# Optimization experiments

Measured on AMD Instinct MI355X. Metric: run time of the kernel, lower is better.

The kernel has to match this reference:

```python
import jax, jax.numpy as jnp
import numpy as np

B, N, K = 4, 2048, 32
CIN, COUT, M = 64, 64, 8
HID = 16
EPS = 1e-5


def setup_inputs() -> dict:
    key = jax.random.key(0)
    ks = jax.random.split(key, 12)
    inp = {
        "grouped_xyz": jax.random.normal(ks[0], (B, 3, N, K), jnp.float32),
        "grouped_dist": jax.random.uniform(ks[1], (B, N, K), jnp.float32),
        "grouped_norm": jax.random.normal(ks[2], (B, 3, N, K), jnp.float32),
        "grouped_angle": jax.random.normal(ks[3], (B, 3, N, K), jnp.float32),
        "feature": jax.random.normal(ks[4], (B, CIN, N, K), jnp.float32),
        # scorenet conv1 (14->16, 1x1, no bias) + BN params
        "w1": jax.random.normal(ks[5], (HID, 14), jnp.float32) * (2.0 / 14) ** 0.5,
        "g1": jnp.ones((HID,), jnp.float32),
        "b1": jnp.zeros((HID,), jnp.float32),
        # scorenet conv2 (16->M, 1x1, with bias, no last bn)
        "w2": jax.random.normal(ks[6], (M, HID), jnp.float32) * (2.0 / HID) ** 0.5,
        "bias2": jnp.zeros((M,), jnp.float32),
        # weight bank: kaiming on (M, CIN, COUT) -> permute -> (CIN, M*COUT)
        "weightbank": (jax.random.normal(ks[7], (M, CIN, COUT), jnp.float32)
                       * (2.0 / CIN) ** 0.5).transpose(1, 0, 2).reshape(CIN, M * COUT),
        # output BN params
        "gamma": jnp.ones((COUT,), jnp.float32),
        "beta": jnp.zeros((COUT,), jnp.float32),
    }
    return inp


def _bn_train(x, gamma, beta):
    # BatchNorm2d in training mode: stats over (B, N, K) per channel (axis=1)
    mean = x.mean(axis=(0, 2, 3), keepdims=True)
    var = x.var(axis=(0, 2, 3), keepdims=True)
    xn = (x - mean) * jax.lax.rsqrt(var + EPS)
    return xn * gamma[None, :, None, None] + beta[None, :, None, None]


def _softmax_one(x, axis):
    # exp(x) / (1 + sum exp(x)), numerically stable
    m = jax.lax.stop_gradient(x.max(axis=axis, keepdims=True))
    e = jnp.exp(x - m)
    return e / (e.sum(axis=axis, keepdims=True) + jnp.exp(-m))


def reference(grouped_xyz, grouped_dist, grouped_norm, grouped_angle, feature,
              w1, g1, b1, w2, bias2, weightbank, gamma, beta):
    # geometric feature build -> (B, 14, N, K)
    center_norm = jnp.broadcast_to(grouped_norm[..., :1], grouped_norm.shape)
    norm_diff = grouped_norm - center_norm
    norm_ed = jnp.linalg.norm(norm_diff, axis=1, keepdims=True)   # (B,1,N,K)
    xyz_ed = jnp.linalg.norm(grouped_xyz, axis=1, keepdims=True)  # (B,1,N,K)
    xyz = jnp.concatenate(
        [grouped_xyz, xyz_ed, grouped_norm, norm_diff, norm_ed, grouped_angle],
        axis=1) / (1.0 + grouped_dist[:, None, :, :])

    # scorenet: 1x1 conv + BN + ReLU, then 1x1 conv + bias, softmax_one over channels
    h = jnp.einsum('oc,bcnk->bonk', w1, xyz)
    h = jax.nn.relu(_bn_train(h, g1, b1))
    s = jnp.einsum('oc,bcnk->bonk', w2, h) + bias2[None, :, None, None]
    scores = _softmax_one(s, axis=1)                 # (B, M, N, K)
    scores = scores.transpose(0, 2, 3, 1)            # (B, N, K, M)

    # weight-bank matmul + score-weighted combine
    feat = feature.transpose(0, 2, 3, 1)             # (B, N, K, CIN)
    out = (feat @ weightbank).reshape(B, N, K, M, COUT)
    out = jnp.einsum('bnkm,bnkmo->bnko', scores, out)  # (B, N, K, COUT)
    out = out.transpose(0, 3, 1, 2)                  # (B, COUT, N, K)

    out = _bn_train(out, gamma, beta)
    return jax.nn.relu(out)
```

## Files before the change

### kernel.cpp

```cpp
#include <hip/hip_runtime.h>
#include <hip/hip_bf16.h>
#include <math.h>

namespace {

constexpr int Kn   = 32;
constexpr int CIN  = 64;
constexpr int COUT = 64;
constexpr int Mn   = 8;
constexpr int HIDn = 16;
constexpr int NK   = 65536;
constexpr int PTOT = 262144;
constexpr float EPSf = 1e-5f;

constexpr int WS_SUM1 = 0;
constexpr int WS_SQ1  = 16;
constexpr int WS_SC1  = 32;
constexpr int WS_SH1  = 48;
constexpr int WS_SUM2 = 64;
constexpr int WS_SQ2  = 128;
constexpr int WS_SC2  = 192;
constexpr int WS_SH2  = 256;
constexpr int WS_TOT  = 320;

typedef short bf16x8 __attribute__((ext_vector_type(8)));
typedef float f32x4  __attribute__((ext_vector_type(4)));

__device__ __forceinline__ short f2bf(float f) {
  union { __hip_bfloat16 h; unsigned short u; } cv;
  cv.h = __float2bfloat16(f);
  return (short)cv.u;
}

__device__ __forceinline__ void geom_h(
    const float* __restrict__ xyz, const float* __restrict__ dist,
    const float* __restrict__ nrm, const float* __restrict__ ang,
    const float* __restrict__ w1, int b, int rem, float h[HIDn]) {
  const int cbase = rem & ~(Kn - 1);
  float x[14];
  const float invd = 1.0f / (1.0f + dist[b * NK + rem]);
  float xe = 0.f, ne = 0.f;
#pragma unroll
  for (int d = 0; d < 3; ++d) {
    const int base = (b * 3 + d) * NK;
    const float gx = xyz[base + rem];
    const float gn = nrm[base + rem];
    const float cn = nrm[base + cbase];
    const float ga = ang[base + rem];
    const float nd = gn - cn;
    x[d] = gx; x[4 + d] = gn; x[7 + d] = nd; x[11 + d] = ga;
    xe += gx * gx; ne += nd * nd;
  }
  x[3]  = sqrtf(xe);
  x[10] = sqrtf(ne);
#pragma unroll
  for (int i = 0; i < 14; ++i) x[i] *= invd;
#pragma unroll
  for (int o = 0; o < HIDn; ++o) {
    float s = 0.f;
#pragma unroll
    for (int c = 0; c < 14; ++c) s = fmaf(w1[o * 14 + c], x[c], s);
    h[o] = s;
  }
}

__global__ __launch_bounds__(512) void k0_zero(float* __restrict__ ws) {
  const int t = threadIdx.x;
  if (t < WS_TOT) ws[t] = 0.f;
}

__global__ __launch_bounds__(256) void k1_stats1(
    const float* __restrict__ xyz, const float* __restrict__ dist,
    const float* __restrict__ nrm, const float* __restrict__ ang,
    const float* __restrict__ w1, float* __restrict__ ws) {
  const int pos = blockIdx.x * 256 + threadIdx.x;
  const int b   = pos >> 16;
  const int rem = pos & (NK - 1);
  float h[HIDn];
  geom_h(xyz, dist, nrm, ang, w1, b, rem, h);

  float v[32];
#pragma unroll
  for (int i = 0; i < 16; ++i) { v[i] = h[i]; v[16 + i] = h[i] * h[i]; }
#pragma unroll
  for (int off = 32; off >= 1; off >>= 1) {
#pragma unroll
    for (int i = 0; i < 32; ++i) v[i] += __shfl_xor(v[i], off);
  }
  const int lane = threadIdx.x & 63;
  const int wid  = threadIdx.x >> 6;
  float mv = 0.f;
#pragma unroll
  for (int i = 0; i < 32; ++i) { if (lane == i) mv = v[i]; }
  __shared__ float red[4][32];
  if (lane < 32) red[wid][lane] = mv;
  __syncthreads();
  if (threadIdx.x < 32) {
    const float tot = red[0][threadIdx.x] + red[1][threadIdx.x] +
                      red[2][threadIdx.x] + red[3][threadIdx.x];
    atomicAdd(&ws[WS_SUM1 + threadIdx.x], tot);
  }
}

__global__ __launch_bounds__(64) void k2_fin1(const float* __restrict__ g1,
                                              const float* __restrict__ b1,
                                              float* __restrict__ ws) {
  const int c = threadIdx.x;
  if (c >= HIDn) return;
  const float inv  = 1.0f / (float)PTOT;
  const float mean = ws[WS_SUM1 + c] * inv;
  const float var  = ws[WS_SQ1 + c] * inv - mean * mean;
  const float sc   = g1[c] * rsqrtf(var + EPSf);
  ws[WS_SC1 + c] = sc;
  ws[WS_SH1 + c] = b1[c] - mean * sc;
}

__global__ __launch_bounds__(512, 4) void k3_mfma(
    const float* __restrict__ xyz, const float* __restrict__ dist,
    const float* __restrict__ nrm, const float* __restrict__ ang,
    const float* __restrict__ feature, const float* __restrict__ w1,
    const float* __restrict__ w2, const float* __restrict__ bias2,
    const float* __restrict__ wb, float* __restrict__ ws,
    float* __restrict__ out) {
  __shared__ short lds_b[16 * 4 * 64 * 8];
  __shared__ float red[8][128];

  const int tid = threadIdx.x;
  const int l   = tid & 63;
  const int w   = tid >> 6;
  const int g   = l >> 4;
  const int row = l & 15;

#pragma unroll
  for (int ff = 0; ff < 8; ++ff) {
    const int fi   = w * 8 + ff;
    const int t    = fi >> 2;
    const int colt = fi & 3;
    const int c    = t * 4 + g;
    const int o    = colt * 16 + row;
    bf16x8 frag;
#pragma unroll
    for (int j = 0; j < 8; ++j) frag[j] = f2bf(wb[c * 512 + j * 64 + o]);
    *reinterpret_cast<bf16x8*>(&lds_b[(fi * 64 + l) * 8]) = frag;
  }

  const int pos0 = blockIdx.x * 256 + w * 32;
  const int myp  = pos0 + (l & 31);
  const int b    = myp >> 16;
  const int rem  = myp & (NK - 1);
  float h[HIDn];
  geom_h(xyz, dist, nrm, ang, w1, b, rem, h);
#pragma unroll
  for (int o = 0; o < HIDn; ++o)
    h[o] = fmaxf(fmaf(h[o], ws[WS_SC1 + o], ws[WS_SH1 + o]), 0.f);
  float s[Mn];
#pragma unroll
  for (int m = 0; m < Mn; ++m) {
    float a = bias2[m];
#pragma unroll
    for (int j = 0; j < HIDn; ++j) a = fmaf(w2[m * HIDn + j], h[j], a);
    s[m] = a;
  }
  float mx = s[0];
#pragma unroll
  for (int m = 1; m < Mn; ++m) mx = fmaxf(mx, s[m]);
  float sc[Mn];
  float ssum = 0.f;
#pragma unroll
  for (int m = 0; m < Mn; ++m) { sc[m] = expf(s[m] - mx); ssum += sc[m]; }
  const float inv = 1.0f / (ssum + expf(-mx));
#pragma unroll
  for (int m = 0; m < Mn; ++m) sc[m] *= inv;

  float scA[Mn], scB[Mn];
#pragma unroll
  for (int m = 0; m < Mn; ++m) {
    scA[m] = __shfl(sc[m], row);
    scB[m] = __shfl(sc[m], row + 16);
  }

  __syncthreads();

  const int bb      = pos0 >> 16;
  const int wav_rem = pos0 & (NK - 1);
  const float* fbase = feature + (size_t)bb * CIN * NK + wav_rem;
  f32x4 acc[2][4];
#pragma unroll
  for (int i = 0; i < 2; ++i)
#pragma unroll
    for (int j = 0; j < 4; ++j) acc[i][j] = (f32x4){0.f, 0.f, 0.f, 0.f};

#pragma unroll
  for (int t = 0; t < 16; ++t) {
    const int c = t * 4 + g;
    const float fA = fbase[c * NK + row];
    const float fB = fbase[c * NK + 16 + row];
    bf16x8 a0, a1;
#pragma unroll
    for (int m = 0; m < Mn; ++m) {
      a0[m] = f2bf(fA * scA[m]);
      a1[m] = f2bf(fB * scB[m]);
    }
#pragma unroll
    for (int ct = 0; ct < 4; ++ct) {
      const bf16x8 bfr =
          *reinterpret_cast<const bf16x8*>(&lds_b[((t * 4 + ct) * 64 + l) * 8]);
      acc[0][ct] = __builtin_amdgcn_mfma_f32_16x16x32_bf16(a0, bfr, acc[0][ct], 0, 0, 0);
      acc[1][ct] = __builtin_amdgcn_mfma_f32_16x16x32_bf16(a1, bfr, acc[1][ct], 0, 0, 0);
    }
  }

  float* obase = out + (size_t)bb * COUT * NK + wav_rem;
#pragma unroll
  for (int tau = 0; tau < 2; ++tau) {
#pragma unroll
    for (int ct = 0; ct < 4; ++ct) {
      const int o = ct * 16 + row;
      *reinterpret_cast<f32x4*>(&obase[(size_t)o * NK + tau * 16 + 4 * g]) =
          acc[tau][ct];
    }
  }

  float s2[4], q2[4];
#pragma unroll
  for (int ct = 0; ct < 4; ++ct) {
    float a = 0.f, q = 0.f;
#pragma unroll
    for (int tau = 0; tau < 2; ++tau)
#pragma unroll
      for (int i = 0; i < 4; ++i) {
        const float v = acc[tau][ct][i];
        a += v; q += v * v;
      }
    s2[ct] = a; q2[ct] = q;
  }
#pragma unroll
  for (int ct = 0; ct < 4; ++ct) {
    s2[ct] += __shfl_xor(s2[ct], 16); s2[ct] += __shfl_xor(s2[ct], 32);
    q2[ct] += __shfl_xor(q2[ct], 16); q2[ct] += __shfl_xor(q2[ct], 32);
  }
  if (l < 16) {
#pragma unroll
    for (int ct = 0; ct < 4; ++ct) {
      red[w][ct * 16 + l]      = s2[ct];
      red[w][64 + ct * 16 + l] = q2[ct];
    }
  }
  __syncthreads();
  if (tid < 128) {
    float tot = 0.f;
#pragma unroll
    for (int ww = 0; ww < 8; ++ww) tot += red[ww][tid];
    atomicAdd(&ws[WS_SUM2 + tid], tot);
  }
}

__global__ __launch_bounds__(64) void k4_fin2(const float* __restrict__ gamma,
                                              const float* __restrict__ beta,
                                              float* __restrict__ ws) {
  const int c = threadIdx.x;
  const float inv  = 1.0f / (float)PTOT;
  const float mean = ws[WS_SUM2 + c] * inv;
  const float var  = ws[WS_SQ2 + c] * inv - mean * mean;
  const float sc   = gamma[c] * rsqrtf(var + EPSf);
  ws[WS_SC2 + c] = sc;
  ws[WS_SH2 + c] = beta[c] - mean * sc;
}

__global__ __launch_bounds__(256) void k5_bn2(float* __restrict__ out,
                                              const float* __restrict__ ws) {
  const int i4 = blockIdx.x * 256 + threadIdx.x;
  const int o  = (i4 >> 14) & 63;
  const float sc = ws[WS_SC2 + o];
  const float sh = ws[WS_SH2 + o];
  float4 v = reinterpret_cast<float4*>(out)[i4];
  v.x = fmaxf(fmaf(v.x, sc, sh), 0.f);
  v.y = fmaxf(fmaf(v.y, sc, sh), 0.f);
  v.z = fmaxf(fmaf(v.z, sc, sh), 0.f);
  v.w = fmaxf(fmaf(v.w, sc, sh), 0.f);
  reinterpret_cast<float4*>(out)[i4] = v;
}

}

extern "C" void kernel_launch(void* const* d_in, const int* in_sizes, int n_in,
                              void* d_out, int out_size, void* d_ws, size_t ws_size,
                              hipStream_t stream) {
  const float* xyz     = (const float*)d_in[0];
  const float* dist    = (const float*)d_in[1];
  const float* nrm     = (const float*)d_in[2];
  const float* ang     = (const float*)d_in[3];
  const float* feature = (const float*)d_in[4];
  const float* w1      = (const float*)d_in[5];
  const float* g1      = (const float*)d_in[6];
  const float* b1      = (const float*)d_in[7];
  const float* w2      = (const float*)d_in[8];
  const float* bias2   = (const float*)d_in[9];
  const float* wb      = (const float*)d_in[10];
  const float* gamma   = (const float*)d_in[11];
  const float* beta    = (const float*)d_in[12];
  float* out = (float*)d_out;
  float* ws  = (float*)d_ws;

  hipLaunchKernelGGL(k0_zero, dim3(1), dim3(512), 0, stream, ws);
  hipLaunchKernelGGL(k1_stats1, dim3(PTOT / 256), dim3(256), 0, stream,
                     xyz, dist, nrm, ang, w1, ws);
  hipLaunchKernelGGL(k2_fin1, dim3(1), dim3(64), 0, stream, g1, b1, ws);
  hipLaunchKernelGGL(k3_mfma, dim3(PTOT / 256), dim3(512), 0, stream,
                     xyz, dist, nrm, ang, feature, w1, w2, bias2, wb, ws, out);
  hipLaunchKernelGGL(k4_fin2, dim3(1), dim3(64), 0, stream, gamma, beta, ws);
  hipLaunchKernelGGL(k5_bn2, dim3((PTOT * COUT / 4) / 256), dim3(256), 0, stream,
                     out, ws);
}
```

Before: 98.68 us.

## Fuse all stages into one persistent kernel with software grid barriers

Replaces the stats1, finalize1, MFMA, finalize2 and BN2 kernels with a single persistent kernel of 256 blocks by 1024 threads. It uses two atomic-counter grid barriers to wait for global BatchNorm statistics, and keeps the MFMA accumulators in registers across the second barrier. The output is normalized and written once, so the separate read-modify-write pass over the 64-channel output and the recomputation of the geometry features are gone. The cost is that every block must be co-resident for the barriers to avoid deadlock, and each thread now holds twice the accumulators, which puts pressure on registers and occupancy.

```diff
diff --git a/kernel.cpp b/kernel.cpp
--- a/kernel.cpp
+++ b/kernel.cpp
@@ -13,15 +13,15 @@
 constexpr int PTOT = 262144;
 constexpr float EPSf = 1e-5f;
 
+constexpr int NBLK = 256;
+constexpr int NTHR = 1024;
+
 constexpr int WS_SUM1 = 0;
 constexpr int WS_SQ1  = 16;
-constexpr int WS_SC1  = 32;
-constexpr int WS_SH1  = 48;
 constexpr int WS_SUM2 = 64;
 constexpr int WS_SQ2  = 128;
-constexpr int WS_SC2  = 192;
-constexpr int WS_SH2  = 256;
-constexpr int WS_TOT  = 320;
+constexpr int WS_BAR  = 192;
+constexpr int WS_TOT  = 256;
 
 typedef short bf16x8 __attribute__((ext_vector_type(8)));
 typedef float f32x4  __attribute__((ext_vector_type(4)));
@@ -30,6 +30,22 @@
   union { __hip_bfloat16 h; unsigned short u; } cv;
   cv.h = __float2bfloat16(f);
   return (short)cv.u;
+}
+
+__device__ __forceinline__ float ws_ld(const float* p) {
+  return __hip_atomic_load(p, __ATOMIC_RELAXED, __HIP_MEMORY_SCOPE_AGENT);
+}
+
+__device__ __forceinline__ void gridbar(int* cnt, int tid, int target) {
+  __syncthreads();
+  if (tid == 0) {
+    __hip_atomic_fetch_add(cnt, 1, __ATOMIC_ACQ_REL, __HIP_MEMORY_SCOPE_AGENT);
+    while (__hip_atomic_load(cnt, __ATOMIC_ACQUIRE,
+                             __HIP_MEMORY_SCOPE_AGENT) < target) {
+      __builtin_amdgcn_s_sleep(8);
+    }
+  }
+  __syncthreads();
 }
 
 __device__ __forceinline__ void geom_h(
@@ -65,65 +81,23 @@
 }
 
 __global__ __launch_bounds__(512) void k0_zero(float* __restrict__ ws) {
-  const int t = threadIdx.x;
-  if (t < WS_TOT) ws[t] = 0.f;
-}
-
-__global__ __launch_bounds__(256) void k1_stats1(
-    const float* __restrict__ xyz, const float* __restrict__ dist,
-    const float* __restrict__ nrm, const float* __restrict__ ang,
-    const float* __restrict__ w1, float* __restrict__ ws) {
-  const int pos = blockIdx.x * 256 + threadIdx.x;
-  const int b   = pos >> 16;
-  const int rem = pos & (NK - 1);
-  float h[HIDn];
-  geom_h(xyz, dist, nrm, ang, w1, b, rem, h);
-
-  float v[32];
-#pragma unroll
-  for (int i = 0; i < 16; ++i) { v[i] = h[i]; v[16 + i] = h[i] * h[i]; }
-#pragma unroll
-  for (int off = 32; off >= 1; off >>= 1) {
-#pragma unroll
-    for (int i = 0; i < 32; ++i) v[i] += __shfl_xor(v[i], off);
-  }
-  const int lane = threadIdx.x & 63;
-  const int wid  = threadIdx.x >> 6;
-  float mv = 0.f;
-#pragma unroll
-  for (int i = 0; i < 32; ++i) { if (lane == i) mv = v[i]; }
-  __shared__ float red[4][32];
-  if (lane < 32) red[wid][lane] = mv;
-  __syncthreads();
-  if (threadIdx.x < 32) {
-    const float tot = red[0][threadIdx.x] + red[1][threadIdx.x] +
-                      red[2][threadIdx.x] + red[3][threadIdx.x];
-    atomicAdd(&ws[WS_SUM1 + threadIdx.x], tot);
-  }
-}
-
-__global__ __launch_bounds__(64) void k2_fin1(const float* __restrict__ g1,
-                                              const float* __restrict__ b1,
-                                              float* __restrict__ ws) {
-  const int c = threadIdx.x;
-  if (c >= HIDn) return;
-  const float inv  = 1.0f / (float)PTOT;
-  const float mean = ws[WS_SUM1 + c] * inv;
-  const float var  = ws[WS_SQ1 + c] * inv - mean * mean;
-  const float sc   = g1[c] * rsqrtf(var + EPSf);
-  ws[WS_SC1 + c] = sc;
-  ws[WS_SH1 + c] = b1[c] - mean * sc;
-}
-
-__global__ __launch_bounds__(512, 4) void k3_mfma(
+  if (threadIdx.x < WS_TOT) ws[threadIdx.x] = 0.f;
+}
+
+__global__ __launch_bounds__(NTHR, 4) void kmain(
     const float* __restrict__ xyz, const float* __restrict__ dist,
     const float* __restrict__ nrm, const float* __restrict__ ang,
     const float* __restrict__ feature, const float* __restrict__ w1,
+    const float* __restrict__ g1, const float* __restrict__ b1,
     const float* __restrict__ w2, const float* __restrict__ bias2,
-    const float* __restrict__ wb, float* __restrict__ ws,
+    const float* __restrict__ wb, const float* __restrict__ gamma,
+    const float* __restrict__ beta, float* __restrict__ ws,
     float* __restrict__ out) {
   __shared__ short lds_b[16 * 4 * 64 * 8];
-  __shared__ float red[8][128];
+  __shared__ float red[16][128];
+  __shared__ float bnp[160];
+
+  int* const bar = (int*)(ws + WS_BAR);
 
   const int tid = threadIdx.x;
   const int l   = tid & 63;
@@ -131,9 +105,14 @@
   const int g   = l >> 4;
   const int row = l & 15;
 
-#pragma unroll
-  for (int ff = 0; ff < 8; ++ff) {
-    const int fi   = w * 8 + ff;
+  const int blk = blockIdx.x;
+  const int pos = blk * NTHR + tid;
+  const int b   = pos >> 16;
+  const int rem = pos & (NK - 1);
+
+#pragma unroll
+  for (int ff = 0; ff < 4; ++ff) {
+    const int fi   = w * 4 + ff;
     const int t    = fi >> 2;
     const int colt = fi & 3;
     const int c    = t * 4 + g;
@@ -144,141 +123,166 @@
     *reinterpret_cast<bf16x8*>(&lds_b[(fi * 64 + l) * 8]) = frag;
   }
 
-  const int pos0 = blockIdx.x * 256 + w * 32;
-  const int myp  = pos0 + (l & 31);
-  const int b    = myp >> 16;
-  const int rem  = myp & (NK - 1);
   float h[HIDn];
   geom_h(xyz, dist, nrm, ang, w1, b, rem, h);
-#pragma unroll
-  for (int o = 0; o < HIDn; ++o)
-    h[o] = fmaxf(fmaf(h[o], ws[WS_SC1 + o], ws[WS_SH1 + o]), 0.f);
-  float s[Mn];
-#pragma unroll
-  for (int m = 0; m < Mn; ++m) {
-    float a = bias2[m];
-#pragma unroll
-    for (int j = 0; j < HIDn; ++j) a = fmaf(w2[m * HIDn + j], h[j], a);
-    s[m] = a;
-  }
-  float mx = s[0];
-#pragma unroll
-  for (int m = 1; m < Mn; ++m) mx = fmaxf(mx, s[m]);
+  {
+    float v[32];
+#pragma unroll
+    for (int i = 0; i < 16; ++i) { v[i] = h[i]; v[16 + i] = h[i] * h[i]; }
+#pragma unroll
+    for (int off = 32; off >= 1; off >>= 1) {
+#pragma unroll
+      for (int i = 0; i < 32; ++i) v[i] += __shfl_xor(v[i], off);
+    }
+    float mv = 0.f;
+#pragma unroll
+    for (int i = 0; i < 32; ++i) { if (l == i) mv = v[i]; }
+    if (l < 32) red[w][l] = mv;
+    __syncthreads();
+    if (tid < 32) {
+      float tot = 0.f;
+#pragma unroll
+      for (int ww = 0; ww < 16; ++ww) tot += red[ww][tid];
+      atomicAdd(&ws[WS_SUM1 + tid], tot);
+    }
+  }
+
+  gridbar(bar, tid, NBLK);
+
+  if (tid < HIDn) {
+    const float inv  = 1.0f / (float)PTOT;
+    const float mean = ws_ld(&ws[WS_SUM1 + tid]) * inv;
+    const float var  = ws_ld(&ws[WS_SQ1 + tid]) * inv - mean * mean;
+    const float s    = g1[tid] * rsqrtf(var + EPSf);
+    bnp[tid]      = s;
+    bnp[16 + tid] = b1[tid] - mean * s;
+  }
+  __syncthreads();
+
   float sc[Mn];
-  float ssum = 0.f;
-#pragma unroll
-  for (int m = 0; m < Mn; ++m) { sc[m] = expf(s[m] - mx); ssum += sc[m]; }
-  const float inv = 1.0f / (ssum + expf(-mx));
-#pragma unroll
-  for (int m = 0; m < Mn; ++m) sc[m] *= inv;
-
-  float scA[Mn], scB[Mn];
-#pragma unroll
-  for (int m = 0; m < Mn; ++m) {
-    scA[m] = __shfl(sc[m], row);
-    scB[m] = __shfl(sc[m], row + 16);
-  }
-
+  {
+#pragma unroll
+    for (int o = 0; o < HIDn; ++o)
+      h[o] = fmaxf(fmaf(h[o], bnp[o], bnp[16 + o]), 0.f);
+    float s[Mn];
+#pragma unroll
+    for (int m = 0; m < Mn; ++m) {
+      float a = bias2[m];
+#pragma unroll
+      for (int j = 0; j < HIDn; ++j) a = fmaf(w2[m * HIDn + j], h[j], a);
+      s[m] = a;
+    }
+    float mx = s[0];
+#pragma unroll
+    for (int m = 1; m < Mn; ++m) mx = fmaxf(mx, s[m]);
+    float ssum = 0.f;
+#pragma unroll
+    for (int m = 0; m < Mn; ++m) { sc[m] = expf(s[m] - mx); ssum += sc[m]; }
+    const float inv = 1.0f / (ssum + expf(-mx));
+#pragma unroll
+    for (int m = 0; m < Mn; ++m) sc[m] *= inv;
+  }
+
+  const int wrem = (blk * NTHR + w * 64) & (NK - 1);
+  const float* fbase = feature + (size_t)b * CIN * NK + wrem;
+  f32x4 acc[4][4];
+#pragma unroll
+  for (int r = 0; r < 4; ++r)
+#pragma unroll
+    for (int j = 0; j < 4; ++j) acc[r][j] = (f32x4){0.f, 0.f, 0.f, 0.f};
+
+#pragma unroll
+  for (int pr = 0; pr < 2; ++pr) {
+    float s0[Mn], s1[Mn];
+#pragma unroll
+    for (int m = 0; m < Mn; ++m) {
+      s0[m] = __shfl(sc[m], pr * 32 + row);
+      s1[m] = __shfl(sc[m], pr * 32 + 16 + row);
+    }
+#pragma unroll
+    for (int t = 0; t < 16; ++t) {
+      const int c = t * 4 + g;
+      const float fA = fbase[c * NK + pr * 32 + row];
+      const float fB = fbase[c * NK + pr * 32 + 16 + row];
+      bf16x8 a0, a1;
+#pragma unroll
+      for (int m = 0; m < Mn; ++m) {
+        a0[m] = f2bf(fA * s0[m]);
+        a1[m] = f2bf(fB * s1[m]);
+      }
+#pragma unroll
+      for (int ct = 0; ct < 4; ++ct) {
+        const bf16x8 bfr = *reinterpret_cast<const bf16x8*>(
+            &lds_b[((t * 4 + ct) * 64 + l) * 8]);
+        acc[pr * 2 + 0][ct] = __builtin_amdgcn_mfma_f32_16x16x32_bf16(
+            a0, bfr, acc[pr * 2 + 0][ct], 0, 0, 0);
+        acc[pr * 2 + 1][ct] = __builtin_amdgcn_mfma_f32_16x16x32_bf16(
+            a1, bfr, acc[pr * 2 + 1][ct], 0, 0, 0);
+      }
+    }
+  }
+
+  {
+    float s2[4], q2[4];
+#pragma unroll
+    for (int ct = 0; ct < 4; ++ct) {
+      float a = 0.f, q = 0.f;
+#pragma unroll
+      for (int r = 0; r < 4; ++r)
+#pragma unroll
+        for (int i = 0; i < 4; ++i) {
+          const float vv = acc[r][ct][i];
+          a += vv; q += vv * vv;
+        }
+      s2[ct] = a; q2[ct] = q;
+    }
+#pragma unroll
+    for (int ct = 0; ct < 4; ++ct) {
+      s2[ct] += __shfl_xor(s2[ct], 16); s2[ct] += __shfl_xor(s2[ct], 32);
+      q2[ct] += __shfl_xor(q2[ct], 16); q2[ct] += __shfl_xor(q2[ct], 32);
+    }
+    if (l < 16) {
+#pragma unroll
+      for (int ct = 0; ct < 4; ++ct) {
+        red[w][ct * 16 + l]      = s2[ct];
+        red[w][64 + ct * 16 + l] = q2[ct];
+      }
+    }
+    __syncthreads();
+    if (tid < 128) {
+      float tot = 0.f;
+#pragma unroll
+      for (int ww = 0; ww < 16; ++ww) tot += red[ww][tid];
+      atomicAdd(&ws[WS_SUM2 + tid], tot);
+    }
+  }
+
+  gridbar(bar, tid, 2 * NBLK);
+
+  if (tid < COUT) {
+    const float inv  = 1.0f / (float)PTOT;
+    const float mean = ws_ld(&ws[WS_SUM2 + tid]) * inv;
+    const float var  = ws_ld(&ws[WS_SQ2 + tid]) * inv - mean * mean;
+    const float s    = gamma[tid] * rsqrtf(var + EPSf);
+    bnp[32 + tid] = s;
+    bnp[96 + tid] = beta[tid] - mean * s;
+  }
   __syncthreads();
 
-  const int bb      = pos0 >> 16;
-  const int wav_rem = pos0 & (NK - 1);
-  const float* fbase = feature + (size_t)bb * CIN * NK + wav_rem;
-  f32x4 acc[2][4];
-#pragma unroll
-  for (int i = 0; i < 2; ++i)
-#pragma unroll
-    for (int j = 0; j < 4; ++j) acc[i][j] = (f32x4){0.f, 0.f, 0.f, 0.f};
-
-#pragma unroll
-  for (int t = 0; t < 16; ++t) {
-    const int c = t * 4 + g;
-    const float fA = fbase[c * NK + row];
-    const float fB = fbase[c * NK + 16 + row];
-    bf16x8 a0, a1;
-#pragma unroll
-    for (int m = 0; m < Mn; ++m) {
-      a0[m] = f2bf(fA * scA[m]);
-      a1[m] = f2bf(fB * scB[m]);
-    }
-#pragma unroll
-    for (int ct = 0; ct < 4; ++ct) {
-      const bf16x8 bfr =
-          *reinterpret_cast<const bf16x8*>(&lds_b[((t * 4 + ct) * 64 + l) * 8]);
-      acc[0][ct] = __builtin_amdgcn_mfma_f32_16x16x32_bf16(a0, bfr, acc[0][ct], 0, 0, 0);
-      acc[1][ct] = __builtin_amdgcn_mfma_f32_16x16x32_bf16(a1, bfr, acc[1][ct], 0, 0, 0);
-    }
-  }
-
-  float* obase = out + (size_t)bb * COUT * NK + wav_rem;
-#pragma unroll
-  for (int tau = 0; tau < 2; ++tau) {
+  float* obase = out + (size_t)b * COUT * NK + wrem;
+#pragma unroll
+  for (int r = 0; r < 4; ++r) {
 #pragma unroll
     for (int ct = 0; ct < 4; ++ct) {
       const int o = ct * 16 + row;
-      *reinterpret_cast<f32x4*>(&obase[(size_t)o * NK + tau * 16 + 4 * g]) =
-          acc[tau][ct];
-    }
-  }
-
-  float s2[4], q2[4];
-#pragma unroll
-  for (int ct = 0; ct < 4; ++ct) {
-    float a = 0.f, q = 0.f;
-#pragma unroll
-    for (int tau = 0; tau < 2; ++tau)
-#pragma unroll
-      for (int i = 0; i < 4; ++i) {
-        const float v = acc[tau][ct][i];
-        a += v; q += v * v;
-      }
-    s2[ct] = a; q2[ct] = q;
-  }
-#pragma unroll
-  for (int ct = 0; ct < 4; ++ct) {
-    s2[ct] += __shfl_xor(s2[ct], 16); s2[ct] += __shfl_xor(s2[ct], 32);
-    q2[ct] += __shfl_xor(q2[ct], 16); q2[ct] += __shfl_xor(q2[ct], 32);
-  }
-  if (l < 16) {
-#pragma unroll
-    for (int ct = 0; ct < 4; ++ct) {
-      red[w][ct * 16 + l]      = s2[ct];
-      red[w][64 + ct * 16 + l] = q2[ct];
-    }
-  }
-  __syncthreads();
-  if (tid < 128) {
-    float tot = 0.f;
-#pragma unroll
-    for (int ww = 0; ww < 8; ++ww) tot += red[ww][tid];
-    atomicAdd(&ws[WS_SUM2 + tid], tot);
-  }
-}
-
-__global__ __launch_bounds__(64) void k4_fin2(const float* __restrict__ gamma,
-                                              const float* __restrict__ beta,
-                                              float* __restrict__ ws) {
-  const int c = threadIdx.x;
-  const float inv  = 1.0f / (float)PTOT;
-  const float mean = ws[WS_SUM2 + c] * inv;
-  const float var  = ws[WS_SQ2 + c] * inv - mean * mean;
-  const float sc   = gamma[c] * rsqrtf(var + EPSf);
-  ws[WS_SC2 + c] = sc;
-  ws[WS_SH2 + c] = beta[c] - mean * sc;
-}
-
-__global__ __launch_bounds__(256) void k5_bn2(float* __restrict__ out,
-                                              const float* __restrict__ ws) {
-  const int i4 = blockIdx.x * 256 + threadIdx.x;
-  const int o  = (i4 >> 14) & 63;
-  const float sc = ws[WS_SC2 + o];
-  const float sh = ws[WS_SH2 + o];
-  float4 v = reinterpret_cast<float4*>(out)[i4];
-  v.x = fmaxf(fmaf(v.x, sc, sh), 0.f);
-  v.y = fmaxf(fmaf(v.y, sc, sh), 0.f);
-  v.z = fmaxf(fmaf(v.z, sc, sh), 0.f);
-  v.w = fmaxf(fmaf(v.w, sc, sh), 0.f);
-  reinterpret_cast<float4*>(out)[i4] = v;
+      const float scl = bnp[32 + o];
+      const float sh  = bnp[96 + o];
+      f32x4 vv = acc[r][ct];
+#pragma unroll
+      for (int i = 0; i < 4; ++i) vv[i] = fmaxf(fmaf(vv[i], scl, sh), 0.f);
+      *reinterpret_cast<f32x4*>(&obase[(size_t)o * NK + r * 16 + 4 * g]) = vv;
+    }
+  }
 }
 
 }
@@ -303,12 +307,7 @@
   float* ws  = (float*)d_ws;
 
   hipLaunchKernelGGL(k0_zero, dim3(1), dim3(512), 0, stream, ws);
-  hipLaunchKernelGGL(k1_stats1, dim3(PTOT / 256), dim3(256), 0, stream,
-                     xyz, dist, nrm, ang, w1, ws);
-  hipLaunchKernelGGL(k2_fin1, dim3(1), dim3(64), 0, stream, g1, b1, ws);
-  hipLaunchKernelGGL(k3_mfma, dim3(PTOT / 256), dim3(512), 0, stream,
-                     xyz, dist, nrm, ang, feature, w1, w2, bias2, wb, ws, out);
-  hipLaunchKernelGGL(k4_fin2, dim3(1), dim3(64), 0, stream, gamma, beta, ws);
-  hipLaunchKernelGGL(k5_bn2, dim3((PTOT * COUT / 4) / 256), dim3(256), 0, stream,
-                     out, ws);
-}
+  hipLaunchKernelGGL(kmain, dim3(NBLK), dim3(NTHR), 0, stream,
+                     xyz, dist, nrm, ang, feature, w1, g1, b1,
+                     w2, bias2, wb, gamma, beta, ws, out);
+}
```

After: 247.3 us. +150.6%, slower.
